# Performance work log

Hardware: AMD Instinct MI355X
Metric: run time of the kernel (lower is better)

## Reference

```python
import jax, jax.numpy as jnp
import numpy as np

BS, SEQ, D_IN, D_OUT = 4, 1024, 1024, 1024
N_SKILLS, RANK = 8, 4
SCALING = 1.0  # lora_alpha / rank, folded into one constant
NEG_INF = -1e38


def setup_inputs() -> dict:
    key = jax.random.key(0)
    ks = jax.random.split(key, 5)
    x = jax.random.normal(ks[0], (BS, SEQ, D_IN), jnp.float32)
    phi = jax.random.normal(ks[1], (D_IN, N_SKILLS), jnp.float32) * 0.02
    lora_a = jax.random.normal(ks[2], (N_SKILLS, D_IN, RANK), jnp.float32) * 0.02
    lora_b = jax.random.normal(ks[3], (N_SKILLS, RANK, D_OUT), jnp.float32) * 0.02
    W = jax.random.normal(ks[4], (D_OUT, D_IN), jnp.float32) * 0.02
    b = jnp.zeros((D_OUT,), jnp.float32)
    # left-padded sequences with an instruction prefix right after the padding
    pad_len = np.array([100, 0, 250, 50])
    inst_len = 300
    pad = np.zeros((BS, SEQ), np.int32)
    inst = np.zeros((BS, SEQ), np.int32)
    for i in range(BS):
        pad[i, pad_len[i]:] = 1
        inst[i, pad_len[i]:pad_len[i] + inst_len] = 1
    return {"x": x, "phi": phi, "lora_a": lora_a, "lora_b": lora_b,
            "W": W, "b": b,
            "inst_mask": jnp.asarray(inst), "pad_mask": jnp.asarray(pad)}


def _causal_prefix_mask(inst_mask, pad_mask):
    # faithful port of create_causal_prefix_mask (padding_side='left')
    bs, seq = inst_mask.shape
    first_one = jnp.argmax(inst_mask, axis=1, keepdims=True)          # [b,1]
    n_ones = jnp.sum(inst_mask, axis=1, keepdims=True)                # [b,1]
    thresh = first_one + n_ones                                       # last_one_idx + 1
    exp = jnp.broadcast_to(thresh, (bs, seq))                         # [b,s]
    inv = jnp.maximum(seq - exp - jnp.arange(seq)[None, :], 0)[:, ::-1]
    m = (exp + inv) * pad_mask                                        # [b,s]
    m3 = m[:, :, None] * pad_mask[:, None, :]                         # [b,s,s]
    ar = jnp.arange(seq)[None, None, :]
    return ar < m3                                                    # bool [b,s,s]


def reference(x, phi, lora_a, lora_b, W, b, inst_mask, pad_mask):
    # router: mixing logits per token per skill
    mw = jnp.einsum('bsd,dn->bsn', x, phi)                            # [b,s,k]
    cm = _causal_prefix_mask(inst_mask, pad_mask)                     # [b,s,s]
    padf = pad_mask.astype(x.dtype)
    # expand over attended positions p, mask, softmax over p
    logits = jnp.where(cm[..., None], mw[:, :, None, :], NEG_INF)     # [b,s,p,k]
    logits = jnp.transpose(logits, (0, 3, 1, 2))                      # [b,k,s,p]
    D = jax.nn.softmax(logits, axis=-1)
    D = D * padf[:, None, :, None]                                    # zero padded query rows
    # token mixing: contract over source tokens (last axis of D)
    input_mixed = jnp.einsum('bsd,bkps->bkpd', x, D)                  # [b,k,s,d]
    # per-skill LoRA (n_splits == 1, q squeezed)
    ar_r = jnp.einsum('bksd,kdr->bskr', input_mixed, lora_a)          # [b,s,k,r]
    ad = jnp.einsum('bskr,krd->bskd', ar_r, lora_b)                   # [b,s,k,d_out]
    # softmax-weighted combine over skills
    C = jax.nn.softmax(mw, axis=-1)
    adapter_out = jnp.einsum('bsk,bskd->bsd', C, ad) * SCALING
    base = jnp.einsum('bsd,od->bso', x, W) + b
    return base + adapter_out
```

## Files before the change

kernel.cpp:

```cpp
#include <hip/hip_runtime.h>
#include <hip/hip_bf16.h>
#include <cstdint>

#define SEQ   1024
#define DOUT  1024
#define KDIM  1024
#define MTOT  4096

typedef __bf16 bf16x8 __attribute__((ext_vector_type(8)));
typedef float  f32x4  __attribute__((ext_vector_type(4)));

__device__ inline unsigned short f2bf(float f) {
  union { float f; unsigned u; } a; a.f = f;
  unsigned r = a.u + 0x7fff + ((a.u >> 16) & 1);
  return (unsigned short)(r >> 16);
}

__device__ inline void gl16(const void* g, void* l) {
  __builtin_amdgcn_global_load_lds((__attribute__((address_space(1))) void*)g,
                                   (__attribute__((address_space(3))) void*)l, 16, 0, 0);
}

__global__ __launch_bounds__(256) void k_mwz(const float* __restrict__ x, unsigned short* __restrict__ xb,
                                             const float* __restrict__ phi, const float* __restrict__ la,
                                             float* __restrict__ mwzP) {
  __shared__ __align__(16) unsigned short Bs[48 * 264];
  int bm = blockIdx.x, ks = blockIdx.y;
  int tid = threadIdx.x, wave = tid >> 6, lane = tid & 63;
  int quad = lane >> 4, lr = lane & 15;

#pragma unroll
  for (int j = 0; j < 16; ++j) {
    int u = j * 256 + tid;
    int row = u >> 6, c4 = u & 63;
    size_t base = (size_t)(bm * 64 + row) * KDIM + ks * 256;
    float4 v = *((const float4*)(x + base) + c4);
    ushort4 o; o.x = f2bf(v.x); o.y = f2bf(v.y); o.z = f2bf(v.z); o.w = f2bf(v.w);
    *((ushort4*)(xb + base) + c4) = o;
  }
  for (int e = tid; e < 48 * 256; e += 256) {
    int r = e >> 8, c = e & 255, d = ks * 256 + c;
    float v;
    if (r < 8)       v = phi[d * 8 + r];
    else if (r < 40) { int kr = r - 8; v = la[(kr >> 2) * 4096 + d * 4 + (kr & 3)]; }
    else             v = 0.f;
    Bs[r * 264 + c] = f2bf(v);
  }
  int arow = bm * 64 + wave * 16 + lr;
  const float* xr = x + (size_t)arow * KDIM + ks * 256 + quad * 8;
  bf16x8 afr[8];
#pragma unroll
  for (int i = 0; i < 8; ++i) {
    float4 a = *(const float4*)(xr + i * 32);
    float4 b = *(const float4*)(xr + i * 32 + 4);
    union { bf16x8 v; unsigned short u[8]; } t;
    t.u[0] = f2bf(a.x); t.u[1] = f2bf(a.y); t.u[2] = f2bf(a.z); t.u[3] = f2bf(a.w);
    t.u[4] = f2bf(b.x); t.u[5] = f2bf(b.y); t.u[6] = f2bf(b.z); t.u[7] = f2bf(b.w);
    afr[i] = t.v;
  }
  __syncthreads();
  f32x4 acc[3];
#pragma unroll
  for (int i = 0; i < 3; ++i) acc[i] = (f32x4){0.f, 0.f, 0.f, 0.f};
  for (int i = 0; i < 8; ++i) {
    int kb = i * 32;
#pragma unroll
    for (int ni = 0; ni < 3; ++ni) {
      bf16x8 bfr = *(const bf16x8*)&Bs[(ni * 16 + lr) * 264 + kb + quad * 8];
      acc[ni] = __builtin_amdgcn_mfma_f32_16x16x32_bf16(afr[i], bfr, acc[ni], 0, 0, 0);
    }
  }
#pragma unroll
  for (int ni = 0; ni < 3; ++ni) {
    int c = ni * 16 + lr;
#pragma unroll
    for (int rg = 0; rg < 4; ++rg) {
      int row = bm * 64 + wave * 16 + quad * 4 + rg;
      if (c < 40) mwzP[(size_t)(ks * 40 + c) * MTOT + row] = acc[ni][rg];
    }
  }
}

__global__ __launch_bounds__(1024) void k_sgp(const float* __restrict__ mwzP,
                                              const int* __restrict__ inst, const int* __restrict__ pad,
                                              const float* __restrict__ W, const float* __restrict__ lb,
                                              unsigned short* __restrict__ Wc, unsigned short* __restrict__ B2T,
                                              unsigned short* __restrict__ gb) {
  int blk = blockIdx.x, tid = threadIdx.x;
  if (blk >= 128) {
    if (blk < 192) {
      size_t base = (size_t)(blk - 128) * 16384;
#pragma unroll
      for (int j = 0; j < 16; ++j) { size_t e = base + j * 1024 + tid; Wc[e] = f2bf(W[e]); }
    } else {
#pragma unroll
      for (int j = 0; j < 32; ++j) {
        int e = j * 1024 + tid;
        B2T[e] = f2bf(lb[(e & 31) * 1024 + (e >> 5)]);
      }
    }
    return;
  }
  int b = blk >> 5, c = blk & 31;
  int wv = tid >> 6, lane = tid & 63;
  __shared__ float wsz[16], wsp[16];
  __shared__ float sv, spc;
  __shared__ int fos[16], nos[16], ths;
  {
    int iv = inst[b * SEQ + tid];
    int fo = iv ? tid : (1 << 30), no = iv;
#pragma unroll
    for (int d = 1; d < 64; d <<= 1) { fo = min(fo, __shfl_xor(fo, d)); no += __shfl_xor(no, d); }
    if (lane == 0) { fos[wv] = fo; nos[wv] = no; }
  }
  __syncthreads();
  if (tid == 0) {
    int F = 1 << 30, N = 0;
#pragma unroll
    for (int i = 0; i < 16; ++i) { F = min(F, fos[i]); N += nos[i]; }
    ths = (N > 0) ? F + N : 0;
  }
  int q = b * SEQ + tid;
  float pm = (float)pad[q];
  float z = 0.f;
#pragma unroll
  for (int s = 0; s < 4; ++s) z += mwzP[(size_t)(s * 40 + 8 + c) * MTOT + q];
  z *= pm;
  float vz = z, vp = pm;
#pragma unroll
  for (int d = 1; d < 64; d <<= 1) {
    float oz = __shfl_up(vz, d), op = __shfl_up(vp, d);
    if (lane >= d) { vz += oz; vp += op; }
  }
  if (lane == 63) { wsz[wv] = vz; wsp[wv] = vp; }
  __syncthreads();
  if (wv == 0 && lane < 16) {
    float oz = wsz[lane], op = wsp[lane], sz = oz, sp = op;
#pragma unroll
    for (int d = 1; d < 16; d <<= 1) {
      float tz = __shfl_up(sz, d), tp = __shfl_up(sp, d);
      if (lane >= d) { sz += tz; sp += tp; }
    }
    wsz[lane] = sz - oz; wsp[lane] = sp - op;
  }
  __syncthreads();
  vz += wsz[wv]; vp += wsp[wv];
  int th = ths;
  if (th > 0 && tid == th - 1) { sv = vz; spc = vp; }
  __syncthreads();
  unsigned short o = 0;
  if (pm != 0.f) {
    bool own = (tid + 1 >= th);
    float Tv  = own ? vz : sv;
    float cnt = own ? vp : spc;
    float C[8], mx = -1e30f;
#pragma unroll
    for (int k = 0; k < 8; ++k) {
      float m = 0.f;
#pragma unroll
      for (int s = 0; s < 4; ++s) m += mwzP[(size_t)(s * 40 + k) * MTOT + q];
      C[k] = m; mx = fmaxf(mx, m);
    }
    float sm = 0.f;
#pragma unroll
    for (int k = 0; k < 8; ++k) { C[k] = __expf(C[k] - mx); sm += C[k]; }
    o = f2bf(C[c >> 2] * Tv / (sm * cnt));
  }
  gb[(size_t)q * 32 + c] = o;
}

__global__ __launch_bounds__(256) void k_gemm(const unsigned short* __restrict__ A,
                                              const unsigned short* __restrict__ Wc,
                                              const unsigned short* __restrict__ gb,
                                              const unsigned short* __restrict__ B2T,
                                              float* __restrict__ out,
                                              const float* __restrict__ bias) {
  __shared__ unsigned short As[128 * 32];
  __shared__ unsigned short Bs[64 * 32];
  int bm = blockIdx.x, bn = blockIdx.y;
  int t = threadIdx.x;
  int wave = t >> 6, lane = t & 63;
  int wr = wave >> 1, wc = wave & 1;
  int quad = lane >> 4, lr = lane & 15;
  f32x4 acc[4][2];
#pragma unroll
  for (int i = 0; i < 4; i++)
#pragma unroll
    for (int j = 0; j < 2; j++) acc[i][j] = (f32x4){0.f, 0.f, 0.f, 0.f};

  const unsigned short* aG = A + (size_t)bm * 128 * KDIM;
  const unsigned short* bG = Wc + (size_t)bn * 64 * KDIM;
  const unsigned short* gA = gb + (size_t)bm * 128 * 32;
  const unsigned short* gB = B2T + (size_t)bn * 64 * 32;
  int r0 = t >> 2, c0 = (t & 3) * 8;

  for (int i = 0; i < 33; ++i) {
    __syncthreads();
    if (i < 32) {
      int kb = i * 32;
      gl16(aG + (size_t)r0 * KDIM + kb + c0,        &As[wave * 512]);
      gl16(aG + (size_t)(r0 + 64) * KDIM + kb + c0, &As[2048 + wave * 512]);
      gl16(bG + (size_t)r0 * KDIM + kb + c0,        &Bs[wave * 512]);
    } else {
      gl16(gA + (size_t)r0 * 32 + c0,        &As[wave * 512]);
      gl16(gA + (size_t)(r0 + 64) * 32 + c0, &As[2048 + wave * 512]);
      gl16(gB + (size_t)r0 * 32 + c0,        &Bs[wave * 512]);
    }
    __syncthreads();
    bf16x8 af[4], bfr[2];
#pragma unroll
    for (int mi = 0; mi < 4; mi++) af[mi]  = *(const bf16x8*)&As[(wr * 64 + mi * 16 + lr) * 32 + quad * 8];
#pragma unroll
    for (int ni = 0; ni < 2; ni++) bfr[ni] = *(const bf16x8*)&Bs[(wc * 32 + ni * 16 + lr) * 32 + quad * 8];
#pragma unroll
    for (int mi = 0; mi < 4; mi++)
#pragma unroll
      for (int ni = 0; ni < 2; ni++)
        acc[mi][ni] = __builtin_amdgcn_mfma_f32_16x16x32_bf16(af[mi], bfr[ni], acc[mi][ni], 0, 0, 0);
  }

#pragma unroll
  for (int mi = 0; mi < 4; mi++) {
#pragma unroll
    for (int ni = 0; ni < 2; ni++) {
      int col = bn * 64 + wc * 32 + ni * 16 + lr;
      float bv = bias[col];
#pragma unroll
      for (int rg = 0; rg < 4; ++rg) {
        int row = bm * 128 + wr * 64 + mi * 16 + quad * 4 + rg;
        out[(size_t)row * DOUT + col] = acc[mi][ni][rg] + bv;
      }
    }
  }
}

extern "C" void kernel_launch(void* const* d_in, const int* in_sizes, int n_in,
                              void* d_out, int out_size, void* d_ws, size_t ws_size,
                              hipStream_t stream) {
  const float* x    = (const float*)d_in[0];
  const float* phi  = (const float*)d_in[1];
  const float* la   = (const float*)d_in[2];
  const float* lb   = (const float*)d_in[3];
  const float* W    = (const float*)d_in[4];
  const float* bias = (const float*)d_in[5];
  const int*   inst = (const int*)d_in[6];
  const int*   pad  = (const int*)d_in[7];
  float* out = (float*)d_out;

  char* ws = (char*)d_ws;
  unsigned short* xb  = (unsigned short*)ws;
  unsigned short* Wc  = (unsigned short*)(ws + 8388608);
  unsigned short* B2T = (unsigned short*)(ws + 10485760);
  float* mwzP = (float*)(ws + 10551296);
  unsigned short* gb  = (unsigned short*)(ws + 13172736);

  hipLaunchKernelGGL(k_mwz,  dim3(64, 4),  dim3(256),  0, stream, x, xb, phi, la, mwzP);
  hipLaunchKernelGGL(k_sgp,  dim3(193),    dim3(1024), 0, stream, mwzP, inst, pad, W, lb, Wc, B2T, gb);
  hipLaunchKernelGGL(k_gemm, dim3(32, 16), dim3(256),  0, stream, xb, Wc, gb, B2T, out, bias);
}
```

Baseline: 131.5 us.

## Vectorize weight conversion, stream router A-tiles from bf16, hoist low-rank MFMA

Three changes. The W and lora_b bf16 conversion in k_sgp is spread across many more blocks, with each thread doing float4 and ushort4 accesses instead of scalar loops over a few blocks. In k_mwz, the A operand is now streamed through LDS from the freshly written bf16 xb buffer rather than reloaded from fp32 x and reconverted, and the B panel uses a per-k-chunk layout. In k_gemm, the extra 33rd low-rank iteration is replaced by a direct global-load MFMA before the main loop, removing one barrier pair and one LDS round trip. A risk is that k_mwz reads xb through global_load_lds immediately after the same block writes it, which depends on those writes being visible after the barrier.

```diff
diff --git a/kernel.cpp b/kernel.cpp
--- a/kernel.cpp
+++ b/kernel.cpp
@@ -24,50 +24,46 @@
 __global__ __launch_bounds__(256) void k_mwz(const float* __restrict__ x, unsigned short* __restrict__ xb,
                                              const float* __restrict__ phi, const float* __restrict__ la,
                                              float* __restrict__ mwzP) {
-  __shared__ __align__(16) unsigned short Bs[48 * 264];
+  __shared__ unsigned short As[64 * 32];
+  __shared__ unsigned short Bp[8 * 48 * 32];
   int bm = blockIdx.x, ks = blockIdx.y;
-  int tid = threadIdx.x, wave = tid >> 6, lane = tid & 63;
+  int t = threadIdx.x, wave = t >> 6, lane = t & 63;
   int quad = lane >> 4, lr = lane & 15;
 
 #pragma unroll
   for (int j = 0; j < 16; ++j) {
-    int u = j * 256 + tid;
+    int u = j * 256 + t;
     int row = u >> 6, c4 = u & 63;
     size_t base = (size_t)(bm * 64 + row) * KDIM + ks * 256;
     float4 v = *((const float4*)(x + base) + c4);
     ushort4 o; o.x = f2bf(v.x); o.y = f2bf(v.y); o.z = f2bf(v.z); o.w = f2bf(v.w);
     *((ushort4*)(xb + base) + c4) = o;
   }
-  for (int e = tid; e < 48 * 256; e += 256) {
-    int r = e >> 8, c = e & 255, d = ks * 256 + c;
+  for (int e = t; e < 48 * 256; e += 256) {
+    int r = e >> 8, dc = e & 255, d = ks * 256 + dc;
     float v;
     if (r < 8)       v = phi[d * 8 + r];
     else if (r < 40) { int kr = r - 8; v = la[(kr >> 2) * 4096 + d * 4 + (kr & 3)]; }
     else             v = 0.f;
-    Bs[r * 264 + c] = f2bf(v);
-  }
-  int arow = bm * 64 + wave * 16 + lr;
-  const float* xr = x + (size_t)arow * KDIM + ks * 256 + quad * 8;
-  bf16x8 afr[8];
-#pragma unroll
-  for (int i = 0; i < 8; ++i) {
-    float4 a = *(const float4*)(xr + i * 32);
-    float4 b = *(const float4*)(xr + i * 32 + 4);
-    union { bf16x8 v; unsigned short u[8]; } t;
-    t.u[0] = f2bf(a.x); t.u[1] = f2bf(a.y); t.u[2] = f2bf(a.z); t.u[3] = f2bf(a.w);
-    t.u[4] = f2bf(b.x); t.u[5] = f2bf(b.y); t.u[6] = f2bf(b.z); t.u[7] = f2bf(b.w);
-    afr[i] = t.v;
-  }
-  __syncthreads();
+    Bp[(dc >> 5) * 1536 + r * 32 + (dc & 31)] = f2bf(v);
+  }
+
+  const unsigned short* aG = xb + (size_t)bm * 64 * KDIM + ks * 256;
+  int r0 = t >> 2, c0 = (t & 3) * 8;
   f32x4 acc[3];
 #pragma unroll
   for (int i = 0; i < 3; ++i) acc[i] = (f32x4){0.f, 0.f, 0.f, 0.f};
-  for (int i = 0; i < 8; ++i) {
-    int kb = i * 32;
+
+  for (int kb = 0; kb < 256; kb += 32) {
+    __syncthreads();
+    gl16(aG + (size_t)r0 * KDIM + kb + c0, &As[wave * 512]);
+    __syncthreads();
+    bf16x8 af = *(const bf16x8*)&As[(wave * 16 + lr) * 32 + quad * 8];
+    const unsigned short* bc = &Bp[(kb >> 5) * 1536];
 #pragma unroll
     for (int ni = 0; ni < 3; ++ni) {
-      bf16x8 bfr = *(const bf16x8*)&Bs[(ni * 16 + lr) * 264 + kb + quad * 8];
-      acc[ni] = __builtin_amdgcn_mfma_f32_16x16x32_bf16(afr[i], bfr, acc[ni], 0, 0, 0);
+      bf16x8 bfr = *(const bf16x8*)&bc[(ni * 16 + lr) * 32 + quad * 8];
+      acc[ni] = __builtin_amdgcn_mfma_f32_16x16x32_bf16(af, bfr, acc[ni], 0, 0, 0);
     }
   }
 #pragma unroll
@@ -88,16 +84,20 @@
                                               unsigned short* __restrict__ gb) {
   int blk = blockIdx.x, tid = threadIdx.x;
   if (blk >= 128) {
-    if (blk < 192) {
-      size_t base = (size_t)(blk - 128) * 16384;
-#pragma unroll
-      for (int j = 0; j < 16; ++j) { size_t e = base + j * 1024 + tid; Wc[e] = f2bf(W[e]); }
+    if (blk < 384) {
+      size_t e4 = (size_t)(blk - 128) * 1024 + tid;
+      float4 v = ((const float4*)W)[e4];
+      ushort4 o; o.x = f2bf(v.x); o.y = f2bf(v.y); o.z = f2bf(v.z); o.w = f2bf(v.w);
+      ((ushort4*)Wc)[e4] = o;
     } else {
-#pragma unroll
-      for (int j = 0; j < 32; ++j) {
-        int e = j * 1024 + tid;
-        B2T[e] = f2bf(lb[(e & 31) * 1024 + (e >> 5)]);
-      }
+      int i = (blk - 384) * 4096 + tid * 4;
+      int n = i >> 5, kr = i & 31;
+      ushort4 o;
+      o.x = f2bf(lb[(kr + 0) * 1024 + n]);
+      o.y = f2bf(lb[(kr + 1) * 1024 + n]);
+      o.z = f2bf(lb[(kr + 2) * 1024 + n]);
+      o.w = f2bf(lb[(kr + 3) * 1024 + n]);
+      *(ushort4*)(B2T + i) = o;
     }
     return;
   }
@@ -188,24 +188,30 @@
 #pragma unroll
     for (int j = 0; j < 2; j++) acc[i][j] = (f32x4){0.f, 0.f, 0.f, 0.f};
 
+  {
+    bf16x8 ga[4], gBf[2];
+#pragma unroll
+    for (int mi = 0; mi < 4; mi++)
+      ga[mi] = *(const bf16x8*)(gb + (size_t)(bm * 128 + wr * 64 + mi * 16 + lr) * 32 + quad * 8);
+#pragma unroll
+    for (int ni = 0; ni < 2; ni++)
+      gBf[ni] = *(const bf16x8*)(B2T + (size_t)(bn * 64 + wc * 32 + ni * 16 + lr) * 32 + quad * 8);
+#pragma unroll
+    for (int mi = 0; mi < 4; mi++)
+#pragma unroll
+      for (int ni = 0; ni < 2; ni++)
+        acc[mi][ni] = __builtin_amdgcn_mfma_f32_16x16x32_bf16(ga[mi], gBf[ni], acc[mi][ni], 0, 0, 0);
+  }
+
   const unsigned short* aG = A + (size_t)bm * 128 * KDIM;
   const unsigned short* bG = Wc + (size_t)bn * 64 * KDIM;
-  const unsigned short* gA = gb + (size_t)bm * 128 * 32;
-  const unsigned short* gB = B2T + (size_t)bn * 64 * 32;
   int r0 = t >> 2, c0 = (t & 3) * 8;
 
-  for (int i = 0; i < 33; ++i) {
-    __syncthreads();
-    if (i < 32) {
-      int kb = i * 32;
-      gl16(aG + (size_t)r0 * KDIM + kb + c0,        &As[wave * 512]);
-      gl16(aG + (size_t)(r0 + 64) * KDIM + kb + c0, &As[2048 + wave * 512]);
-      gl16(bG + (size_t)r0 * KDIM + kb + c0,        &Bs[wave * 512]);
-    } else {
-      gl16(gA + (size_t)r0 * 32 + c0,        &As[wave * 512]);
-      gl16(gA + (size_t)(r0 + 64) * 32 + c0, &As[2048 + wave * 512]);
-      gl16(gB + (size_t)r0 * 32 + c0,        &Bs[wave * 512]);
-    }
+  for (int kb = 0; kb < KDIM; kb += 32) {
+    __syncthreads();
+    gl16(aG + (size_t)r0 * KDIM + kb + c0,        &As[wave * 512]);
+    gl16(aG + (size_t)(r0 + 64) * KDIM + kb + c0, &As[2048 + wave * 512]);
+    gl16(bG + (size_t)r0 * KDIM + kb + c0,        &Bs[wave * 512]);
     __syncthreads();
     bf16x8 af[4], bfr[2];
 #pragma unroll
@@ -255,6 +261,6 @@
   unsigned short* gb  = (unsigned short*)(ws + 13172736);
 
   hipLaunchKernelGGL(k_mwz,  dim3(64, 4),  dim3(256),  0, stream, x, xb, phi, la, mwzP);
-  hipLaunchKernelGGL(k_sgp,  dim3(193),    dim3(1024), 0, stream, mwzP, inst, pad, W, lb, Wc, B2T, gb);
+  hipLaunchKernelGGL(k_sgp,  dim3(392),    dim3(1024), 0, stream, mwzP, inst, pad, W, lb, Wc, B2T, gb);
   hipLaunchKernelGGL(k_gemm, dim3(32, 16), dim3(256),  0, stream, xb, Wc, gb, B2T, out, bias);
 }
```

After: 122.0 us. 7.2% less time.
